# Kernel optimization log

Hardware: AMD Instinct MI355X
Metric: run time of the kernel (lower is better)

The kernel has to match this reference:

```python
import jax, jax.numpy as jnp
import numpy as np

B, T, C = 2, 2048, 1024
E = 8            # num_experts
K = 2            # num_active (top-k)
H = 4 * C        # expert hidden dim


def setup_inputs() -> dict:
    key = jax.random.key(0)
    ks = jax.random.split(key, 8)
    s = 0.02
    return {
        "x": jax.random.normal(ks[0], (B, T, C), dtype=jnp.float32),
        "Wg": jax.random.normal(ks[1], (C, E), dtype=jnp.float32) * s,
        "bg": jnp.zeros((E,), dtype=jnp.float32),
        "W1": jax.random.normal(ks[2], (E, C, H), dtype=jnp.float32) * s,
        "b1": jnp.zeros((E, H), dtype=jnp.float32),
        "W2": jax.random.normal(ks[3], (E, H, C), dtype=jnp.float32) * s,
        "b2": jnp.zeros((E, C), dtype=jnp.float32),
    }


def reference(x, Wg, bg, W1, b1, W2, b2):
    Bs, Ts, Cs = x.shape
    x_flat = x.reshape(-1, Cs)                       # [N, C]
    gate_logits = x_flat @ Wg + bg                   # [N, E]
    gates = jax.nn.softmax(gate_logits, axis=-1)
    w, idx = jax.lax.top_k(gates, K)                 # [N, K]
    w = w / jnp.sum(w, axis=-1, keepdims=True)
    # combine[n, e] = sum_k w[n,k] * (idx[n,k] == e); zero for unrouted experts,
    # so weighting the dense per-expert output reproduces the masked scatter-add.
    combine = jnp.sum(jax.nn.one_hot(idx, E, dtype=x.dtype) * w[..., None], axis=1)  # [N, E]
    out = jnp.zeros_like(x_flat)
    for e in range(E):  # small fixed expert loop; GEMM-dominated
        h = jax.nn.gelu(x_flat @ W1[e] + b1[e], approximate=False)  # [N, H]
        y = h @ W2[e] + b2[e]                                       # [N, C]
        out = out + y * combine[:, e:e + 1]
    return out.reshape(Bs, Ts, Cs)
```

## Files before the change

### kernel.cpp

```cpp
#include <hip/hip_runtime.h>
#include <hip/hip_bf16.h>
#include <math.h>

#define NTOK  4096
#define CDIM  1024
#define HDIM  4096
#define NEXP  8
#define TOPK  2

using short8 = __attribute__((ext_vector_type(8))) short;
using f32x4  = __attribute__((ext_vector_type(4))) float;
using us4    = __attribute__((ext_vector_type(4))) unsigned short;

__device__ inline ushort f2bf(float f) {
    uint32_t u = __builtin_bit_cast(uint32_t, f);
    uint32_t r = (u + 0x7FFFu + ((u >> 16) & 1u)) >> 16;
    return (ushort)r;
}

__device__ __forceinline__ void gl_lds16(const void* g, void* l) {
    __builtin_amdgcn_global_load_lds(
        (const __attribute__((address_space(1))) void*)(void*)g,
        (__attribute__((address_space(3))) void*)l, 16, 0, 0);
}

__global__ __launch_bounds__(256)
void gate_kernel(const float* __restrict__ x, const float* __restrict__ Wg,
                 const float* __restrict__ bg, int* __restrict__ counts,
                 int* __restrict__ tlist, float* __restrict__ wslot,
                 ushort* __restrict__ xbf) {
    int wave = threadIdx.x >> 6, lane = threadIdx.x & 63;
    int t = blockIdx.x * 4 + wave;
    const float* xr = x + (size_t)t * CDIM;

    float acc[NEXP];
#pragma unroll
    for (int e = 0; e < NEXP; e++) acc[e] = 0.f;

#pragma unroll
    for (int i = 0; i < CDIM / 64; i++) {
        int c = lane + 64 * i;
        float xv = xr[c];
        xbf[(size_t)t * CDIM + c] = f2bf(xv);
        const float* wr = Wg + (size_t)c * NEXP;
#pragma unroll
        for (int e = 0; e < NEXP; e++) acc[e] += xv * wr[e];
    }
#pragma unroll
    for (int e = 0; e < NEXP; e++) {
        float v = acc[e];
        for (int off = 32; off > 0; off >>= 1) v += __shfl_xor(v, off);
        acc[e] = v + bg[e];
    }
    if (lane == 0) {
        int i1 = 0; float m1 = acc[0];
#pragma unroll
        for (int e = 1; e < NEXP; e++) if (acc[e] > m1) { m1 = acc[e]; i1 = e; }
        int i2 = -1; float m2 = -1e30f;
#pragma unroll
        for (int e = 0; e < NEXP; e++) if (e != i1 && acc[e] > m2) { m2 = acc[e]; i2 = e; }
        float w0 = 1.f / (1.f + expf(m2 - m1));
        float w1 = 1.f - w0;
        int p0 = atomicAdd(&counts[i1], 1);
        tlist[i1 * NTOK + p0] = t * 2;
        int p1 = atomicAdd(&counts[i2], 1);
        tlist[i2 * NTOK + p1] = t * 2 + 1;
        wslot[t * 2]     = w0;
        wslot[t * 2 + 1] = w1;
    }
}

__global__ __launch_bounds__(256)
void transpose_kernel(const float* __restrict__ in, ushort* __restrict__ out,
                      int R, int Ccols) {
    __shared__ float tile[64][68];
    int e = blockIdx.z;
    const float* src = in + (size_t)e * R * Ccols;
    ushort* dst = out + (size_t)e * Ccols * R;
    int c0 = blockIdx.x * 64, r0 = blockIdx.y * 64;
    int tid = threadIdx.x;
    int tx = tid & 15, ty = tid >> 4;
#pragma unroll
    for (int j = 0; j < 4; j++) {
        float4 v = *(const float4*)&src[(size_t)(r0 + ty + 16 * j) * Ccols + c0 + tx * 4];
        *(float4*)&tile[ty + 16 * j][tx * 4] = v;
    }
    __syncthreads();
#pragma unroll
    for (int j = 0; j < 4; j++) {
        int c = ty + 16 * j;
        us4 o;
#pragma unroll
        for (int i = 0; i < 4; i++) o[i] = f2bf(tile[tx * 4 + i][c]);
        *(us4*)&dst[(size_t)(c0 + c) * R + r0 + tx * 4] = o;
    }
}

template<int GELU, int OUTBF16>
__global__ __launch_bounds__(256)
void moe_gemm(const ushort* __restrict__ A, const ushort* __restrict__ Bt,
              const float* __restrict__ bias, const int* __restrict__ tlist,
              const int* __restrict__ counts, void* __restrict__ Out,
              int K, int N, int ashift) {
    int e = blockIdx.z;
    int cnt = counts[e];
    int m0 = blockIdx.y * 128;
    if (m0 >= cnt) return;
    int n0 = blockIdx.x * 128;

    __shared__ ushort As[128 * 32];
    __shared__ ushort Bs[128 * 32];
    __shared__ int rowv[128];

    int tid = threadIdx.x;
    if (tid < 128) {
        int r = m0 + tid;
        rowv[tid] = tlist[e * NTOK + (r < cnt ? r : cnt - 1)];
    }
    __syncthreads();

    const ushort* Be = Bt + (size_t)e * N * K;

    f32x4 acc[4][4] = {};

    int lane = tid & 63, w = tid >> 6;
    int wm = (w >> 1) * 64, wn = (w & 1) * 64;
    int quad = lane >> 4, l16 = lane & 15;

    int srow = tid >> 2;
    int scol = (tid & 3) * 8;

    for (int kt = 0; kt < K; kt += 32) {
#pragma unroll
        for (int s = 0; s < 2; s++) {
            int row = srow + s * 64;
            const ushort* ap = A + (size_t)(rowv[row] >> ashift) * K + kt + scol;
            gl_lds16(ap, &As[(w * 16 + s * 64) * 32]);
            const ushort* bp = Be + (size_t)(n0 + row) * K + kt + scol;
            gl_lds16(bp, &Bs[(w * 16 + s * 64) * 32]);
        }
        __syncthreads();

        short8 a[4], b[4];
#pragma unroll
        for (int mt = 0; mt < 4; mt++)
            a[mt] = *(short8*)&As[(wm + mt * 16 + l16) * 32 + quad * 8];
#pragma unroll
        for (int nt = 0; nt < 4; nt++)
            b[nt] = *(short8*)&Bs[(wn + nt * 16 + l16) * 32 + quad * 8];
#pragma unroll
        for (int mt = 0; mt < 4; mt++)
#pragma unroll
            for (int nt = 0; nt < 4; nt++)
                acc[mt][nt] = __builtin_amdgcn_mfma_f32_16x16x32_bf16(
                    a[mt], b[nt], acc[mt][nt], 0, 0, 0);
        __syncthreads();
    }

    float* outF = (float*)Out;
    ushort* outH = (ushort*)Out;
    const float* be = bias + (size_t)e * N;
#pragma unroll
    for (int mt = 0; mt < 4; mt++) {
#pragma unroll
        for (int r = 0; r < 4; r++) {
            int lrow = wm + mt * 16 + quad * 4 + r;
            if (m0 + lrow < cnt) {
                int v = rowv[lrow];
                size_t base = (size_t)v * N;
#pragma unroll
                for (int nt = 0; nt < 4; nt++) {
                    int col = n0 + wn + nt * 16 + l16;
                    float val = acc[mt][nt][r] + be[col];
                    if (GELU) val = 0.5f * val * (1.0f + erff(val * 0.70710678118654752f));
                    if (OUTBF16) outH[base + col] = f2bf(val);
                    else         outF[base + col] = val;
                }
            }
        }
    }
}

__global__ __launch_bounds__(256)
void combine_kernel(const float* __restrict__ y, const float* __restrict__ wslot,
                    float* __restrict__ out) {
    int idx = blockIdx.x * 256 + threadIdx.x;
    int c4 = idx & (CDIM / 4 - 1);
    int t = idx >> 8;
    float w0 = wslot[2 * t], w1 = wslot[2 * t + 1];
    const float4* y0 = (const float4*)(y + (size_t)(2 * t) * CDIM);
    const float4* y1 = (const float4*)(y + (size_t)(2 * t + 1) * CDIM);
    float4 a = y0[c4], b = y1[c4], o;
    o.x = w0 * a.x + w1 * b.x;
    o.y = w0 * a.y + w1 * b.y;
    o.z = w0 * a.z + w1 * b.z;
    o.w = w0 * a.w + w1 * b.w;
    ((float4*)(out + (size_t)t * CDIM))[c4] = o;
}

extern "C" void kernel_launch(void* const* d_in, const int* in_sizes, int n_in,
                              void* d_out, int out_size, void* d_ws, size_t ws_size,
                              hipStream_t stream) {
    const float* x  = (const float*)d_in[0];
    const float* Wg = (const float*)d_in[1];
    const float* bg = (const float*)d_in[2];
    const float* W1 = (const float*)d_in[3];
    const float* b1 = (const float*)d_in[4];
    const float* W2 = (const float*)d_in[5];
    const float* b2 = (const float*)d_in[6];
    float* out = (float*)d_out;
    char* ws = (char*)d_ws;

    size_t off = 0;
    int*    counts = (int*)(ws + off);    off += 256;
    int*    tlist  = (int*)(ws + off);    off += (size_t)NEXP * NTOK * 4;
    float*  wslot  = (float*)(ws + off);  off += (size_t)NTOK * TOPK * 4;
    ushort* xbf    = (ushort*)(ws + off); off += (size_t)NTOK * CDIM * 2;
    ushort* WT     = (ushort*)(ws + off); off += (size_t)NEXP * CDIM * HDIM * 2;
    ushort* h      = (ushort*)(ws + off); off += (size_t)NTOK * TOPK * HDIM * 2;
    float*  y      = (float*)(ws + off);  off += (size_t)NTOK * TOPK * CDIM * 4;

    hipMemsetAsync(counts, 0, NEXP * sizeof(int), stream);

    gate_kernel<<<NTOK / 4, 256, 0, stream>>>(x, Wg, bg, counts, tlist, wslot, xbf);

    transpose_kernel<<<dim3(HDIM / 64, CDIM / 64, NEXP), 256, 0, stream>>>(
        W1, WT, CDIM, HDIM);

    moe_gemm<1, 1><<<dim3(HDIM / 128, NTOK / 128, NEXP), 256, 0, stream>>>(
        xbf, WT, b1, tlist, counts, (void*)h, CDIM, HDIM, 1);

    transpose_kernel<<<dim3(CDIM / 64, HDIM / 64, NEXP), 256, 0, stream>>>(
        W2, WT, HDIM, CDIM);

    moe_gemm<0, 0><<<dim3(CDIM / 128, NTOK / 128, NEXP), 256, 0, stream>>>(
        h, WT, b2, tlist, counts, (void*)y, HDIM, CDIM, 0);

    combine_kernel<<<(NTOK * CDIM / 4) / 256, 256, 0, stream>>>(y, wslot, out);
}
```

Baseline: 701.5 us.

## Double-buffer MoE GEMM LDS tiles with XOR swizzle and occupancy hint

The MoE GEMM now double-buffers its A and B LDS tiles, so the global-to-LDS load of the next k-step is issued before the MFMAs of the current step run, leaving one barrier per step. It also XOR-swizzles the 16-byte chunk layout within each tile row to cut LDS bank conflicts on the short8 fragment reads. A launch_bounds minimum of 3 blocks per CU is added to cap register use. The transpose tile padding changes to 65 and its float4 LDS store is split into scalar stores, aimed at conflict-free column reads.

```diff
diff --git a/kernel.cpp b/kernel.cpp
--- a/kernel.cpp
+++ b/kernel.cpp
@@ -73,7 +73,7 @@
 __global__ __launch_bounds__(256)
 void transpose_kernel(const float* __restrict__ in, ushort* __restrict__ out,
                       int R, int Ccols) {
-    __shared__ float tile[64][68];
+    __shared__ float tile[64][65];
     int e = blockIdx.z;
     const float* src = in + (size_t)e * R * Ccols;
     ushort* dst = out + (size_t)e * Ccols * R;
@@ -82,8 +82,12 @@
     int tx = tid & 15, ty = tid >> 4;
 #pragma unroll
     for (int j = 0; j < 4; j++) {
-        float4 v = *(const float4*)&src[(size_t)(r0 + ty + 16 * j) * Ccols + c0 + tx * 4];
-        *(float4*)&tile[ty + 16 * j][tx * 4] = v;
+        int r = ty + 16 * j;
+        float4 v = *(const float4*)&src[(size_t)(r0 + r) * Ccols + c0 + tx * 4];
+        tile[r][tx * 4 + 0] = v.x;
+        tile[r][tx * 4 + 1] = v.y;
+        tile[r][tx * 4 + 2] = v.z;
+        tile[r][tx * 4 + 3] = v.w;
     }
     __syncthreads();
 #pragma unroll
@@ -97,7 +101,7 @@
 }
 
 template<int GELU, int OUTBF16>
-__global__ __launch_bounds__(256)
+__global__ __launch_bounds__(256, 3)
 void moe_gemm(const ushort* __restrict__ A, const ushort* __restrict__ Bt,
               const float* __restrict__ bias, const int* __restrict__ tlist,
               const int* __restrict__ counts, void* __restrict__ Out,
@@ -108,8 +112,8 @@
     if (m0 >= cnt) return;
     int n0 = blockIdx.x * 128;
 
-    __shared__ ushort As[128 * 32];
-    __shared__ ushort Bs[128 * 32];
+    __shared__ ushort As[2][128 * 32];
+    __shared__ ushort Bs[2][128 * 32];
     __shared__ int rowv[128];
 
     int tid = threadIdx.x;
@@ -121,41 +125,59 @@
 
     const ushort* Be = Bt + (size_t)e * N * K;
 
-    f32x4 acc[4][4] = {};
-
     int lane = tid & 63, w = tid >> 6;
     int wm = (w >> 1) * 64, wn = (w & 1) * 64;
     int quad = lane >> 4, l16 = lane & 15;
 
-    int srow = tid >> 2;
-    int scol = (tid & 3) * 8;
-
-    for (int kt = 0; kt < K; kt += 32) {
-#pragma unroll
-        for (int s = 0; s < 2; s++) {
-            int row = srow + s * 64;
-            const ushort* ap = A + (size_t)(rowv[row] >> ashift) * K + kt + scol;
-            gl_lds16(ap, &As[(w * 16 + s * 64) * 32]);
-            const ushort* bp = Be + (size_t)(n0 + row) * K + kt + scol;
-            gl_lds16(bp, &Bs[(w * 16 + s * 64) * 32]);
-        }
-        __syncthreads();
-
+    int srow   = tid >> 2;
+    int schunk = (tid & 3) ^ ((tid >> 3) & 3);
+    const ushort* pa0 = A  + (size_t)(rowv[srow]      >> ashift) * K + schunk * 8;
+    const ushort* pa1 = A  + (size_t)(rowv[srow + 64] >> ashift) * K + schunk * 8;
+    const ushort* pb0 = Be + (size_t)(n0 + srow)      * K + schunk * 8;
+    const ushort* pb1 = Be + (size_t)(n0 + srow + 64) * K + schunk * 8;
+
+    int swr  = quad ^ ((l16 >> 1) & 3);
+    int aidx = (wm + l16) * 32 + swr * 8;
+    int bidx = (wn + l16) * 32 + swr * 8;
+
+    f32x4 acc[4][4] = {};
+
+    auto STAGE = [&](int buf) {
+        gl_lds16(pa0, &As[buf][(w * 16) * 32]);
+        gl_lds16(pa1, &As[buf][(w * 16 + 64) * 32]);
+        gl_lds16(pb0, &Bs[buf][(w * 16) * 32]);
+        gl_lds16(pb1, &Bs[buf][(w * 16 + 64) * 32]);
+        pa0 += 32; pa1 += 32; pb0 += 32; pb1 += 32;
+    };
+    auto COMPUTE = [&](int buf) {
         short8 a[4], b[4];
 #pragma unroll
-        for (int mt = 0; mt < 4; mt++)
-            a[mt] = *(short8*)&As[(wm + mt * 16 + l16) * 32 + quad * 8];
-#pragma unroll
-        for (int nt = 0; nt < 4; nt++)
-            b[nt] = *(short8*)&Bs[(wn + nt * 16 + l16) * 32 + quad * 8];
+        for (int mt = 0; mt < 4; mt++) a[mt] = *(short8*)&As[buf][aidx + mt * 512];
+#pragma unroll
+        for (int nt = 0; nt < 4; nt++) b[nt] = *(short8*)&Bs[buf][bidx + nt * 512];
 #pragma unroll
         for (int mt = 0; mt < 4; mt++)
 #pragma unroll
             for (int nt = 0; nt < 4; nt++)
                 acc[mt][nt] = __builtin_amdgcn_mfma_f32_16x16x32_bf16(
                     a[mt], b[nt], acc[mt][nt], 0, 0, 0);
+    };
+
+    int nsteps = K >> 5;
+    STAGE(0);
+    __syncthreads();
+    for (int i = 0; i < nsteps - 2; i += 2) {
+        STAGE(1);
+        COMPUTE(0);
         __syncthreads();
-    }
+        STAGE(0);
+        COMPUTE(1);
+        __syncthreads();
+    }
+    STAGE(1);
+    COMPUTE(0);
+    __syncthreads();
+    COMPUTE(1);
 
     float* outF = (float*)Out;
     ushort* outH = (ushort*)Out;
```

Measured after the change: 707.9 us. Within noise of the previous version (+0.9%).
